# Kernel optimization log

Hardware: AMD Instinct MI355X
Metric: run time of the kernel (lower is better)

The kernel has to match this reference:

```python
import jax, jax.numpy as jnp
import numpy as np
import math

B, S, HID, H = 4, 1024, 1024, 16
DH = HID // H

def setup_inputs() -> dict:
    key = jax.random.key(0)
    ks = jax.random.split(key, 16)
    inp = {
        'q': jax.random.normal(ks[0], (B, S, HID), jnp.float32),
        'k': jax.random.normal(ks[1], (B, S, HID), jnp.float32),
        'v': jax.random.normal(ks[2], (B, S, HID), jnp.float32),
        'k_b': jax.random.normal(ks[3], (B, S, HID), jnp.float32),
        'mask': jax.random.randint(ks[4], (B, S), 0, 2, jnp.int32),
    }
    sc = 1.0 / math.sqrt(HID)
    names = ['Wq', 'Wk', 'Wv', 'Wkb', 'Wo']
    for i, n in enumerate(names):
        inp[n] = jax.random.normal(ks[5 + i], (HID, HID), jnp.float32) * sc
        inp['b' + n[1:]] = jnp.zeros((HID,), jnp.float32)
    return inp

def _split_heads(x):
    # [B,S,HID] -> [B,H,S,DH]
    return x.reshape(B, S, H, DH).transpose(0, 2, 1, 3)

def reference(q, k, v, k_b, mask, Wq, bq, Wk, bk, Wv, bv, Wkb, bkb, Wo, bo):
    qh = _split_heads(q @ Wq.T + bq)
    kh = _split_heads(k @ Wk.T + bk)
    vh = _split_heads(v @ Wv.T + bv)
    kbh = _split_heads(k_b @ Wkb.T + bkb)
    scale = 1.0 / math.sqrt(3 * DH)
    # Q@K^T + Q@Kb^T == Q@(K+Kb)^T
    corr = jnp.einsum('bhsd,bhtd->bhst', qh, kh + kbh) * scale
    # mask[b,j] broadcast over heads and query positions
    corr = jnp.where(mask[:, None, None, :] == 0, jnp.float32(-1e9), corr)
    prob = jax.nn.softmax(corr, axis=-1)  # dropout p=0 (eval)
    hidden = jnp.einsum('bhst,bhtd->bhsd', prob, vh)
    hidden = hidden.transpose(0, 2, 1, 3).reshape(B, S, HID)
    return hidden @ Wo.T + bo
```

## Files before the change

kernel.cpp:

```cpp
#include <hip/hip_runtime.h>
#include <hip/hip_bf16.h>
#include <stdint.h>

#define B_   4
#define S_   1024
#define HID_ 1024
#define H_   16
#define DH_  64

typedef short bf16x8 __attribute__((ext_vector_type(8)));
typedef float f32x4  __attribute__((ext_vector_type(4)));
typedef unsigned int u32;
typedef unsigned short u16;

typedef u32 __attribute__((address_space(1))) as1_u32;
typedef u32 __attribute__((address_space(3))) as3_u32;

__device__ __forceinline__ f32x4 mfma16(bf16x8 a, bf16x8 b, f32x4 c) {
  return __builtin_amdgcn_mfma_f32_16x16x32_bf16(a, b, c, 0, 0, 0);
}

__device__ __forceinline__ void gload16(const void* g, void* l) {
  __builtin_amdgcn_global_load_lds((const as1_u32*)g, (as3_u32*)l, 16, 0, 0);
}

__device__ __forceinline__ u16 f2bf(float f) {
  __hip_bfloat16 h = __float2bfloat16(f);
  union { __hip_bfloat16 h; u16 u; } cv; cv.h = h; return cv.u;
}

__device__ __forceinline__ u32 cvtpk(float lo, float hi) {
  u32 r;
  asm("v_cvt_pk_bf16_f32 %0, %1, %2" : "=v"(r) : "v"(lo), "v"(hi));
  return r;
}

template<int NC>
__device__ __forceinline__ void stage_tile(const u16* __restrict__ src, char* smem, int bo,
                                           int tid, int w) {
  #pragma unroll
  for (int is = 0; is < NC; ++is) {
    int o = is * 4096 + tid * 16;
    int row = o >> 7, ch = (o >> 4) & 7;
    gload16(src + (size_t)row * HID_ + ((ch ^ (row & 7)) * 8),
            smem + bo + is * 4096 + w * 1024);
  }
}

__global__ __launch_bounds__(256) void cvt_all(
    const float* a0, const float* a1, const float* a2, const float* a3,
    const float* w0, const float* w1, const float* w2, const float* w3, const float* w4,
    u16* da0, u16* da1, u16* da2, u16* da3,
    u16* dw0, u16* dw1, u16* dw2, u16* dw3, u16* dw4) {
  int bb = blockIdx.x;
  const float* s; u16* d; size_t i;
  if (bb < 8192) {
    int t = bb * 256 + threadIdx.x;
    int sel = t >> 19;
    i = (size_t)(t & 524287) * 8;
    if (sel == 0)      { s = a0; d = da0; }
    else if (sel == 1) { s = a1; d = da1; }
    else if (sel == 2) { s = a2; d = da2; }
    else               { s = a3; d = da3; }
  } else {
    int t = (bb - 8192) * 256 + threadIdx.x;
    int sel = t >> 17;
    i = (size_t)(t & 131071) * 8;
    if (sel == 0)      { s = w0; d = dw0; }
    else if (sel == 1) { s = w1; d = dw1; }
    else if (sel == 2) { s = w2; d = dw2; }
    else if (sel == 3) { s = w3; d = dw3; }
    else               { s = w4; d = dw4; }
  }
  float4 v0 = *(const float4*)(s + i);
  float4 v1 = *(const float4*)(s + i + 4);
  uint4 r;
  r.x = cvtpk(v0.x, v0.y);
  r.y = cvtpk(v0.z, v0.w);
  r.z = cvtpk(v1.x, v1.y);
  r.w = cvtpk(v1.z, v1.w);
  *(uint4*)(d + i) = r;
}

__global__ __launch_bounds__(256, 3) void gemm_proj(
    const u16* __restrict__ qbf, const u16* __restrict__ Wqbf,
    const u16* __restrict__ kbf, const u16* __restrict__ Wkbf,
    const u16* __restrict__ kbbf, const u16* __restrict__ Wkbbf,
    const u16* __restrict__ vbf, const u16* __restrict__ Wvbf,
    const float* __restrict__ bq, const float* __restrict__ bk,
    const float* __restrict__ bkb, const float* __restrict__ bv,
    u16* __restrict__ Qp, u16* __restrict__ KKp, u16* __restrict__ Vtp) {
  __shared__ __align__(16) char smem[49152];
  const int tid = threadIdx.x;
  const int lane = tid & 63, w = tid >> 6;
  const int g = lane >> 4, ql = lane & 15;
  const int wm = w >> 1, wn = w & 1;
  const int xr = ql & 7;
  const int xcd = blockIdx.x & 7, idx = blockIdx.x >> 3;
  const int unit = (idx < 64) ? 0 : (idx < 128) ? 1 : 2;
  const int id = xcd * 64 + (idx & 63);
  const int m0 = (id >> 4) * 128;
  const int n0 = (id & 15) * 64;

  const u16 *A0, *W0, *A1, *W1;
  int nkt;
  if (unit == 0)      { A0 = kbf; W0 = Wkbf; A1 = kbbf; W1 = Wkbbf; nkt = 32; }
  else if (unit == 1) { A0 = qbf; W0 = Wqbf; A1 = qbf;  W1 = Wqbf;  nkt = 16; }
  else                { A0 = vbf; W0 = Wvbf; A1 = vbf;  W1 = Wvbf;  nkt = 16; }

  f32x4 acc[4][2];
  #pragma unroll
  for (int mi = 0; mi < 4; ++mi)
    #pragma unroll
    for (int ni = 0; ni < 2; ++ni) acc[mi][ni] = f32x4{0.f, 0.f, 0.f, 0.f};

  stage_tile<4>(A0 + (size_t)m0 * HID_, smem, 0, tid, w);
  stage_tile<2>(W0 + (size_t)n0 * HID_, smem, 16384, tid, w);

  #pragma unroll 1
  for (int kt = 0; kt < nkt; ++kt) {
    const int boA = (kt & 1) ? 24576 : 0;
    const int boW = (kt & 1) ? 40960 : 16384;
    if (kt < nkt - 1) {
      int kn = kt + 1;
      const u16* As = (kn < 16) ? A0 : A1;
      const u16* Ws = (kn < 16) ? W0 : W1;
      int kk = (kn & 15) * 64;
      stage_tile<4>(As + (size_t)m0 * HID_ + kk, smem, boA ^ 24576, tid, w);
      stage_tile<2>(Ws + (size_t)n0 * HID_ + kk, smem, boW ^ (16384 ^ 40960), tid, w);
      asm volatile("s_waitcnt vmcnt(6)" ::: "memory");
    } else {
      asm volatile("s_waitcnt vmcnt(0)" ::: "memory");
    }
    __builtin_amdgcn_s_barrier();
    const char* ab = smem + boA;
    const char* wb = smem + boW;
    bf16x8 af[4][2], bfv[2][2];
    #pragma unroll
    for (int mi = 0; mi < 4; ++mi)
      #pragma unroll
      for (int c = 0; c < 2; ++c) {
        int row = wm * 64 + mi * 16 + ql;
        af[mi][c] = *(const bf16x8*)(ab + row * 128 + (((c * 4 + g) ^ xr) * 16));
      }
    #pragma unroll
    for (int ni = 0; ni < 2; ++ni)
      #pragma unroll
      for (int c = 0; c < 2; ++c) {
        int row = wn * 32 + ni * 16 + ql;
        bfv[ni][c] = *(const bf16x8*)(wb + row * 128 + (((c * 4 + g) ^ xr) * 16));
      }
    __builtin_amdgcn_s_setprio(1);
    #pragma unroll
    for (int c = 0; c < 2; ++c)
      #pragma unroll
      for (int mi = 0; mi < 4; ++mi)
        #pragma unroll
        for (int ni = 0; ni < 2; ++ni)
          acc[mi][ni] = mfma16(af[mi][c], bfv[ni][c], acc[mi][ni]);
    __builtin_amdgcn_s_setprio(0);
    __builtin_amdgcn_s_barrier();
  }

  if (unit != 2) {
    u16* outp = (unit == 0) ? KKp : Qp;
    const float osc = (unit == 1) ? 0.07216878364870322f * 1.44269504088896340f : 1.f;
    #pragma unroll
    for (int ni = 0; ni < 2; ++ni) {
      int n = n0 + wn * 32 + ni * 16 + ql;
      float bs = (unit == 0) ? (bk[n] + bkb[n]) : bq[n];
      #pragma unroll
      for (int mi = 0; mi < 4; ++mi)
        #pragma unroll
        for (int i = 0; i < 4; ++i) {
          int m = m0 + wm * 64 + mi * 16 + g * 4 + i;
          outp[(size_t)m * HID_ + n] = f2bf((acc[mi][ni][i] + bs) * osc);
        }
    }
  } else {
    char* tp = smem + w * 4096;
    #pragma unroll
    for (int ni = 0; ni < 2; ++ni) {
      int n = n0 + wn * 32 + ni * 16 + ql;
      float bs = bv[n];
      #pragma unroll
      for (int mi = 0; mi < 4; ++mi)
        #pragma unroll
        for (int i = 0; i < 4; ++i) {
          int nl = ni * 16 + ql;
          int ml = mi * 16 + g * 4 + i;
          *(u16*)(tp + nl * 128 + (((ml >> 3) ^ (nl & 7)) * 16) + (ml & 7) * 2) =
              f2bf(acc[mi][ni][i] + bs);
        }
    }
    __syncthreads();
    int r = lane >> 1, half = lane & 1;
    int n = n0 + wn * 32 + r;
    int h = n >> 6, dh = n & 63;
    int b = m0 >> 10;
    int bh = b * H_ + h;
    u16* orow = Vtp + (((size_t)(bh * DH_ + dh)) << 10) + (m0 & 1023) + wm * 64 + half * 32;
    #pragma unroll
    for (int j = 0; j < 4; ++j) {
      uint4 val = *(const uint4*)(tp + r * 128 + (((half * 4 + j) ^ (r & 7)) * 16));
      *(uint4*)(orow + j * 8) = val;
    }
  }
}

__global__ __launch_bounds__(256, 3) void gemm_o(const u16* __restrict__ A0, const u16* __restrict__ W0,
                                                 const float* __restrict__ bias0, float* __restrict__ outp) {
  __shared__ __align__(16) char smem[49152];
  const int tid = threadIdx.x;
  const int lane = tid & 63, w = tid >> 6;
  const int g = lane >> 4, ql = lane & 15;
  const int wm = w >> 1, wn = w & 1;
  const int logical = (blockIdx.x & 7) * 64 + (blockIdx.x >> 3);
  const int m0 = (logical >> 4) * 128;
  const int n0 = (logical & 15) * 64;
  const int xr = ql & 7;

  f32x4 acc[4][2];
  #pragma unroll
  for (int mi = 0; mi < 4; ++mi)
    #pragma unroll
    for (int ni = 0; ni < 2; ++ni) acc[mi][ni] = f32x4{0.f, 0.f, 0.f, 0.f};

  stage_tile<4>(A0 + (size_t)m0 * HID_, smem, 0, tid, w);
  stage_tile<2>(W0 + (size_t)n0 * HID_, smem, 16384, tid, w);

  #pragma unroll 1
  for (int kt = 0; kt < 16; ++kt) {
    const int boA = (kt & 1) ? 24576 : 0;
    const int boW = (kt & 1) ? 40960 : 16384;
    if (kt < 15) {
      int kk = (kt + 1) * 64;
      stage_tile<4>(A0 + (size_t)m0 * HID_ + kk, smem, boA ^ 24576, tid, w);
      stage_tile<2>(W0 + (size_t)n0 * HID_ + kk, smem, boW ^ (16384 ^ 40960), tid, w);
      asm volatile("s_waitcnt vmcnt(6)" ::: "memory");
    } else {
      asm volatile("s_waitcnt vmcnt(0)" ::: "memory");
    }
    __builtin_amdgcn_s_barrier();
    const char* ab = smem + boA;
    const char* wb = smem + boW;
    bf16x8 af[4][2], bfv[2][2];
    #pragma unroll
    for (int mi = 0; mi < 4; ++mi)
      #pragma unroll
      for (int c = 0; c < 2; ++c) {
        int row = wm * 64 + mi * 16 + ql;
        af[mi][c] = *(const bf16x8*)(ab + row * 128 + (((c * 4 + g) ^ xr) * 16));
      }
    #pragma unroll
    for (int ni = 0; ni < 2; ++ni)
      #pragma unroll
      for (int c = 0; c < 2; ++c) {
        int row = wn * 32 + ni * 16 + ql;
        bfv[ni][c] = *(const bf16x8*)(wb + row * 128 + (((c * 4 + g) ^ xr) * 16));
      }
    __builtin_amdgcn_s_setprio(1);
    #pragma unroll
    for (int c = 0; c < 2; ++c)
      #pragma unroll
      for (int mi = 0; mi < 4; ++mi)
        #pragma unroll
        for (int ni = 0; ni < 2; ++ni)
          acc[mi][ni] = mfma16(af[mi][c], bfv[ni][c], acc[mi][ni]);
    __builtin_amdgcn_s_setprio(0);
    __builtin_amdgcn_s_barrier();
  }

  #pragma unroll
  for (int ni = 0; ni < 2; ++ni) {
    int n = n0 + wn * 32 + ni * 16 + ql;
    float bs = bias0[n];
    #pragma unroll
    for (int mi = 0; mi < 4; ++mi)
      #pragma unroll
      for (int i = 0; i < 4; ++i) {
        int m = m0 + wm * 64 + mi * 16 + g * 4 + i;
        outp[(size_t)m * HID_ + n] = acc[mi][ni][i] + bs;
      }
  }
}

__global__ __launch_bounds__(512, 6) void attn(const u16* __restrict__ Qp, const u16* __restrict__ KKp,
                                               const u16* __restrict__ Vt, const int* __restrict__ mask,
                                               u16* __restrict__ hidden) {
  __shared__ __align__(16) char smem[53248];
  const int tid = threadIdx.x;
  const int lane = tid & 63, w = tid >> 6;
  const int g = lane >> 4, ql = lane & 15;
  const int bid = blockIdx.x;
  const int bh = (bid & 7) * 8 + ((bid >> 3) & 7);
  const int qt = bid >> 6;
  const int b = bh >> 4, h = bh & 15;
  const int q0 = qt * 128;
  const int xr = ql & 7;

  {
    int o = tid * 16;
    int row = o >> 7, ch = (o >> 4) & 7;
    gload16(KKp + (size_t)(b * S_ + row) * HID_ + h * DH_ + ((ch ^ (row & 7)) * 8),
            smem + w * 1024);
    gload16(Vt + (size_t)(bh * DH_ + row) * S_ + ((ch ^ (row & 7)) * 8),
            smem + 8192 + w * 1024);
  }
  {
    int2 mv2 = *(const int2*)(mask + b * S_ + tid * 2);
    float2 f;
    f.x = mv2.x ? 0.f : -1e9f;
    f.y = mv2.y ? 0.f : -1e9f;
    *(float2*)(smem + 49152 + tid * 8) = f;
  }

  const u16* qrow = Qp + (size_t)(b * S_ + q0 + w * 16 + ql) * HID_ + h * DH_;
  bf16x8 qb0 = *(const bf16x8*)(qrow + g * 8);
  bf16x8 qb1 = *(const bf16x8*)(qrow + 32 + g * 8);

  f32x4 oacc[4];
  #pragma unroll
  for (int d = 0; d < 4; ++d) oacc[d] = f32x4{0.f, 0.f, 0.f, 0.f};
  float m_run = -1e30f, l_run = 0.f;
  char* pbase = smem + 32768 + w * 2048 + ql * 128;
  const char* madd_l = smem + 49152;

  __syncthreads();

  int pb = 0;
  #pragma unroll 1
  for (int it = 0; it < 16; ++it) {
    const int k0 = it * 64;
    if (it < 15) {
      const int k0s = k0 + 64;
      const int bo = (pb ^ 1) * 16384;
      int o = tid * 16;
      int row = o >> 7, ch = (o >> 4) & 7;
      gload16(KKp + (size_t)(b * S_ + k0s + row) * HID_ + h * DH_ + ((ch ^ (row & 7)) * 8),
              smem + bo + w * 1024);
      gload16(Vt + (size_t)(bh * DH_ + row) * S_ + k0s + ((ch ^ (row & 7)) * 8),
              smem + bo + 8192 + w * 1024);
      asm volatile("s_waitcnt vmcnt(2)" ::: "memory");
    } else {
      asm volatile("s_waitcnt vmcnt(0)" ::: "memory");
    }
    __builtin_amdgcn_s_barrier();

    const char* kb_ = smem + pb * 16384;
    const char* vb_ = smem + pb * 16384 + 8192;

    float sv[4][4];
    #pragma unroll
    for (int t = 0; t < 4; ++t) {
      const char* krow = kb_ + (16 * t + ql) * 128;
      bf16x8 ka0 = *(const bf16x8*)(krow + ((g ^ xr) * 16));
      bf16x8 ka1 = *(const bf16x8*)(krow + (((4 + g) ^ xr) * 16));
      f32x4 st = mfma16(ka0, qb0, f32x4{0.f, 0.f, 0.f, 0.f});
      st = mfma16(ka1, qb1, st);
      f32x4 md = *(const f32x4*)(madd_l + (k0 + 16 * t + 4 * g) * 4);
      sv[t][0] = st[0] + md[0];
      sv[t][1] = st[1] + md[1];
      sv[t][2] = st[2] + md[2];
      sv[t][3] = st[3] + md[3];
    }
    float mloc = sv[0][0];
    #pragma unroll
    for (int t = 0; t < 4; ++t)
      #pragma unroll
      for (int i = 0; i < 4; ++i) mloc = fmaxf(mloc, sv[t][i]);
    mloc = fmaxf(mloc, __shfl_xor(mloc, 16, 64));
    mloc = fmaxf(mloc, __shfl_xor(mloc, 32, 64));
    if (__any(mloc > m_run + 10.f)) {
      float mnew = fmaxf(m_run, mloc);
      float alpha = __builtin_amdgcn_exp2f(m_run - mnew);
      l_run *= alpha;
      #pragma unroll
      for (int d = 0; d < 4; ++d) oacc[d] *= alpha;
      m_run = mnew;
    }
    float rsum = 0.f;
    float pvs[4][4];
    #pragma unroll
    for (int t = 0; t < 4; ++t)
      #pragma unroll
      for (int i = 0; i < 4; ++i) {
        float p = __builtin_amdgcn_exp2f(sv[t][i] - m_run);
        pvs[t][i] = p; rsum += p;
      }
    rsum += __shfl_xor(rsum, 16, 64);
    rsum += __shfl_xor(rsum, 32, 64);
    l_run += rsum;

    #pragma unroll
    for (int t = 0; t < 4; ++t) {
      uint2 pw;
      pw.x = cvtpk(pvs[t][0], pvs[t][1]);
      pw.y = cvtpk(pvs[t][2], pvs[t][3]);
      *(uint2*)(pbase + (((4 * t + g) ^ (2 * xr)) * 8)) = pw;
    }
    #pragma unroll
    for (int c = 0; c < 2; ++c) {
      bf16x8 pf = *(const bf16x8*)(pbase + (((c * 4 + g) ^ xr) * 16));
      #pragma unroll
      for (int d = 0; d < 4; ++d) {
        bf16x8 va = *(const bf16x8*)(vb_ + (16 * d + ql) * 128 + (((c * 4 + g) ^ xr) * 16));
        oacc[d] = mfma16(va, pf, oacc[d]);
      }
    }
    __builtin_amdgcn_s_barrier();
    pb ^= 1;
  }

  float inv = 1.0f / l_run;
  char* ep = smem + w * 2304;
  #pragma unroll
  for (int d = 0; d < 4; ++d)
    #pragma unroll
    for (int i = 0; i < 4; ++i)
      *(u16*)(ep + ql * 144 + (16 * d + 4 * g + i) * 2) = f2bf(oacc[d][i] * inv);
  __syncthreads();
  int r = lane >> 2, cc = lane & 3;
  const char* erow = smem + w * 2304 + r * 144 + cc * 32;
  uint4 v0 = *(const uint4*)erow;
  uint4 v1 = *(const uint4*)(erow + 16);
  u16* orow = hidden + (size_t)(b * S_ + q0 + w * 16 + r) * HID_ + h * DH_ + cc * 16;
  *(uint4*)orow = v0;
  *(uint4*)(orow + 8) = v1;
}

extern "C" void kernel_launch(void* const* d_in, const int* in_sizes, int n_in,
                              void* d_out, int out_size, void* d_ws, size_t ws_size,
                              hipStream_t stream) {
  (void)in_sizes; (void)n_in; (void)out_size; (void)ws_size;
  const float* q    = (const float*)d_in[0];
  const float* k    = (const float*)d_in[1];
  const float* v    = (const float*)d_in[2];
  const float* kb   = (const float*)d_in[3];
  const int*   mask = (const int*)  d_in[4];
  const float* Wq   = (const float*)d_in[5];
  const float* bq   = (const float*)d_in[6];
  const float* Wk   = (const float*)d_in[7];
  const float* bk   = (const float*)d_in[8];
  const float* Wv   = (const float*)d_in[9];
  const float* bv   = (const float*)d_in[10];
  const float* Wkb  = (const float*)d_in[11];
  const float* bkb  = (const float*)d_in[12];
  const float* Wo   = (const float*)d_in[13];
  const float* bo   = (const float*)d_in[14];

  char* ws = (char*)d_ws;
  const size_t MB = 1024 * 1024;
  u16* qbf   = (u16*)(ws + 0 * MB);
  u16* kbf   = (u16*)(ws + 8 * MB);
  u16* vbf   = (u16*)(ws + 16 * MB);
  u16* kbbf  = (u16*)(ws + 24 * MB);
  u16* Wqbf  = (u16*)(ws + 32 * MB);
  u16* Wkbf  = (u16*)(ws + 34 * MB);
  u16* Wvbf  = (u16*)(ws + 36 * MB);
  u16* Wkbbf = (u16*)(ws + 38 * MB);
  u16* Wobf  = (u16*)(ws + 40 * MB);
  u16* Qp    = (u16*)(ws + 42 * MB);
  u16* KKp   = (u16*)(ws + 50 * MB);
  u16* Vtp   = (u16*)(ws + 58 * MB);
  u16* hid   = (u16*)(ws + 66 * MB);

  cvt_all<<<10752, 256, 0, stream>>>(q, k, v, kb, Wq, Wk, Wv, Wkb, Wo,
                                     qbf, kbf, vbf, kbbf, Wqbf, Wkbf, Wvbf, Wkbbf, Wobf);
  gemm_proj<<<1536, 256, 0, stream>>>(qbf, Wqbf, kbf, Wkbf, kbbf, Wkbbf, vbf, Wvbf,
                                      bq, bk, bkb, bv, Qp, KKp, Vtp);
  attn<<<512, 512, 0, stream>>>(Qp, KKp, Vtp, mask, hid);
  gemm_o<<<512, 256, 0, stream>>>(hid, Wobf, bo, (float*)d_out);
}
```

Before: 116.1 us.

## Triple-buffer K/V tiles in attention kernel with two-ahead prefetch

```diff
diff --git a/kernel.cpp b/kernel.cpp
--- a/kernel.cpp
+++ b/kernel.cpp
@@ -288,7 +288,7 @@
 __global__ __launch_bounds__(512, 6) void attn(const u16* __restrict__ Qp, const u16* __restrict__ KKp,
                                                const u16* __restrict__ Vt, const int* __restrict__ mask,
                                                u16* __restrict__ hidden) {
-  __shared__ __align__(16) char smem[53248];
+  __shared__ __align__(16) char smem[69632];
   const int tid = threadIdx.x;
   const int lane = tid & 63, w = tid >> 6;
   const int g = lane >> 4, ql = lane & 15;
@@ -298,21 +298,21 @@
   const int b = bh >> 4, h = bh & 15;
   const int q0 = qt * 128;
   const int xr = ql & 7;
-
-  {
-    int o = tid * 16;
-    int row = o >> 7, ch = (o >> 4) & 7;
-    gload16(KKp + (size_t)(b * S_ + row) * HID_ + h * DH_ + ((ch ^ (row & 7)) * 8),
-            smem + w * 1024);
-    gload16(Vt + (size_t)(bh * DH_ + row) * S_ + ((ch ^ (row & 7)) * 8),
-            smem + 8192 + w * 1024);
-  }
+  const int o = tid * 16;
+  const int srow = o >> 7, sch = (o >> 4) & 7;
+  const size_t kgbase = (size_t)(b * S_ + srow) * HID_ + h * DH_ + ((sch ^ (srow & 7)) * 8);
+  const size_t vgbase = (size_t)(bh * DH_ + srow) * S_ + ((sch ^ (srow & 7)) * 8);
+
+  gload16(KKp + kgbase, smem + w * 1024);
+  gload16(Vt + vgbase, smem + 8192 + w * 1024);
+  gload16(KKp + kgbase + (size_t)64 * HID_, smem + 16384 + w * 1024);
+  gload16(Vt + vgbase + 64, smem + 16384 + 8192 + w * 1024);
   {
     int2 mv2 = *(const int2*)(mask + b * S_ + tid * 2);
     float2 f;
     f.x = mv2.x ? 0.f : -1e9f;
     f.y = mv2.y ? 0.f : -1e9f;
-    *(float2*)(smem + 49152 + tid * 8) = f;
+    *(float2*)(smem + 65536 + tid * 8) = f;
   }
 
   const u16* qrow = Qp + (size_t)(b * S_ + q0 + w * 16 + ql) * HID_ + h * DH_;
@@ -323,32 +323,30 @@
   #pragma unroll
   for (int d = 0; d < 4; ++d) oacc[d] = f32x4{0.f, 0.f, 0.f, 0.f};
   float m_run = -1e30f, l_run = 0.f;
-  char* pbase = smem + 32768 + w * 2048 + ql * 128;
-  const char* madd_l = smem + 49152;
+  char* pbase = smem + 49152 + w * 2048 + ql * 128;
+  const char* madd_l = smem + 65536;
 
   __syncthreads();
 
-  int pb = 0;
+  int cur = 0, st = 2;
   #pragma unroll 1
   for (int it = 0; it < 16; ++it) {
     const int k0 = it * 64;
-    if (it < 15) {
-      const int k0s = k0 + 64;
-      const int bo = (pb ^ 1) * 16384;
-      int o = tid * 16;
-      int row = o >> 7, ch = (o >> 4) & 7;
-      gload16(KKp + (size_t)(b * S_ + k0s + row) * HID_ + h * DH_ + ((ch ^ (row & 7)) * 8),
-              smem + bo + w * 1024);
-      gload16(Vt + (size_t)(bh * DH_ + row) * S_ + k0s + ((ch ^ (row & 7)) * 8),
-              smem + bo + 8192 + w * 1024);
+    if (it < 14) {
+      const int k0s = k0 + 128;
+      const int bo = st * 16384;
+      gload16(KKp + kgbase + (size_t)k0s * HID_, smem + bo + w * 1024);
+      gload16(Vt + vgbase + k0s, smem + bo + 8192 + w * 1024);
+      asm volatile("s_waitcnt vmcnt(4)" ::: "memory");
+    } else if (it == 14) {
       asm volatile("s_waitcnt vmcnt(2)" ::: "memory");
     } else {
       asm volatile("s_waitcnt vmcnt(0)" ::: "memory");
     }
     __builtin_amdgcn_s_barrier();
 
-    const char* kb_ = smem + pb * 16384;
-    const char* vb_ = smem + pb * 16384 + 8192;
+    const char* kb_ = smem + cur * 16384;
+    const char* vb_ = smem + cur * 16384 + 8192;
 
     float sv[4][4];
     #pragma unroll
@@ -356,13 +354,13 @@
       const char* krow = kb_ + (16 * t + ql) * 128;
       bf16x8 ka0 = *(const bf16x8*)(krow + ((g ^ xr) * 16));
       bf16x8 ka1 = *(const bf16x8*)(krow + (((4 + g) ^ xr) * 16));
-      f32x4 st = mfma16(ka0, qb0, f32x4{0.f, 0.f, 0.f, 0.f});
-      st = mfma16(ka1, qb1, st);
+      f32x4 stv = mfma16(ka0, qb0, f32x4{0.f, 0.f, 0.f, 0.f});
+      stv = mfma16(ka1, qb1, stv);
       f32x4 md = *(const f32x4*)(madd_l + (k0 + 16 * t + 4 * g) * 4);
-      sv[t][0] = st[0] + md[0];
-      sv[t][1] = st[1] + md[1];
-      sv[t][2] = st[2] + md[2];
-      sv[t][3] = st[3] + md[3];
+      sv[t][0] = stv[0] + md[0];
+      sv[t][1] = stv[1] + md[1];
+      sv[t][2] = stv[2] + md[2];
+      sv[t][3] = stv[3] + md[3];
     }
     float mloc = sv[0][0];
     #pragma unroll
@@ -409,7 +407,8 @@
       }
     }
     __builtin_amdgcn_s_barrier();
-    pb ^= 1;
+    cur = (cur == 2) ? 0 : cur + 1;
+    st  = (st == 2) ? 0 : st + 1;
   }
 
   float inv = 1.0f / l_run;
```

Result: faster. 113.7 us (-2.0%).
